# Kernel tuning notes

Measured on AMD Instinct MI355X. Metric: run time of the kernel, lower is better.

## Reference

```python
import jax, jax.numpy as jnp
import numpy as np

NUM_ITERS = 3

def squash(s, axis=-1):
    # standard capsule squash: ||s||^2/(1+||s||^2) * s/||s||
    sq = jnp.sum(s * s, axis=axis, keepdims=True)
    norm = jnp.sqrt(sq)
    return (sq / (1.0 + sq)) * (s / norm)

def setup_inputs() -> dict:
    key = jax.random.key(0)
    kx, kw = jax.random.split(key)
    B, I, k, l, O = 512, 1152, 8, 16, 7
    x = jax.random.normal(kx, (B, I, k), dtype=jnp.float32)
    w = jax.random.normal(kw, (I, k, l, O), dtype=jnp.float32)
    return {"x": x, "w": w}

def reference(x, w):
    # x: [B, I, k]; w: [I, k, l, O]
    u_hat = jnp.einsum('BIk,IklO->BIlO', x, w)            # [B, I, l, O]
    I, _, l, _ = w.shape
    b_ij = jnp.zeros((I, l), dtype=u_hat.dtype)
    v_j = None
    for _ in range(NUM_ITERS):
        c_ij = jax.nn.softmax(b_ij, axis=0)               # softmax over I
        s_j = jnp.einsum('Il,BIlO->BlO', c_ij, u_hat)     # [B, l, O]
        v_j = jnp.transpose(squash(s_j), (0, 2, 1))       # [B, O, l]
        u_vj = jnp.einsum('BOl,BIlO->BIl', v_j, u_hat).mean(axis=0)  # [I, l]
        b_ij = b_ij + u_vj
    return v_j
```

## Files before the change

kernel.cpp:

```cpp
#include <hip/hip_runtime.h>
#include <hip/hip_bf16.h>


#define NB 512
#define NI 1152
#define NLO 112
#define NIK 9216
#define NPAD 128

typedef __attribute__((ext_vector_type(8))) short bf16x8;
typedef __attribute__((ext_vector_type(4))) float f32x4;

__device__ __forceinline__ ushort f2bf(float f) {
    __hip_bfloat16 h = __float2bfloat16(f);
    return *(ushort*)&h;
}

__device__ __forceinline__ void conv_x_body(const float* __restrict__ x,
                                            ushort* __restrict__ xbf,
                                            ushort* __restrict__ xT, int bid) {
    __shared__ ushort tile[64][68];
    int kg = bid % 144, bg = bid / 144;
    int k0 = kg * 64, b0 = bg * 64;
    int t = threadIdx.x;
    for (int e = t; e < 1024; e += 256) {
        int r = e >> 4, c4 = (e & 15) * 4;
        float4 f = *(const float4*)&x[(size_t)(b0 + r) * NIK + k0 + c4];
        ushort4 u = { f2bf(f.x), f2bf(f.y), f2bf(f.z), f2bf(f.w) };
        *(ushort4*)&xbf[(size_t)(b0 + r) * NIK + k0 + c4] = u;
        tile[r][c4] = u.x; tile[r][c4 + 1] = u.y; tile[r][c4 + 2] = u.z; tile[r][c4 + 3] = u.w;
    }
    __syncthreads();
    for (int e = t; e < 1024; e += 256) {
        int kr = e >> 4, c4 = (e & 15) * 4;
        ushort4 u = { tile[c4][kr], tile[c4 + 1][kr], tile[c4 + 2][kr], tile[c4 + 3][kr] };
        *(ushort4*)&xT[(size_t)(k0 + kr) * NB + b0 + c4] = u;
    }
}

__global__ __launch_bounds__(256) void prep0(const float* __restrict__ x,
                                             ushort* __restrict__ xbf,
                                             ushort* __restrict__ xT,
                                             const float* __restrict__ w,
                                             ushort* __restrict__ wcTp,
                                             float* __restrict__ Z) {
    if (blockIdx.x < 1152) { conv_x_body(x, xbf, xT, blockIdx.x); return; }
    __shared__ ushort tile[NPAD][66];
    int t = threadIdx.x;
    int ik0 = (blockIdx.x - 1152) * 64;
    if (blockIdx.x == 1152 && t < 48) Z[t] = (t < 16) ? 1.0f : 0.0f;
    const float cv = 1.0f / 1152.0f;
    for (int e = t; e < 8192; e += 256) {
        int ikl = e >> 7, np = e & 127;
        int l = np >> 3, o = np & 7;
        float wv = (o < 7) ? w[(size_t)(ik0 + ikl) * NLO + l * 7 + o] : 0.f;
        tile[np][ikl] = f2bf(cv * wv);
    }
    __syncthreads();
    for (int e = t; e < 8192; e += 256) {
        int np = e >> 6, ikl = e & 63;
        wcTp[(size_t)np * NIK + ik0 + ikl] = tile[np][ikl];
    }
}

__global__ __launch_bounds__(1024) void sq_gemm(const ushort* __restrict__ xbf,
                                                const ushort* __restrict__ wcTp,
                                                const float* __restrict__ Zit,
                                                ushort* __restrict__ vT,
                                                float* __restrict__ out, int wout) {
    __shared__ float sp[16][16][16];
    __shared__ float ss[16][16];
    __shared__ float facs[16][2];
    __shared__ float zi[2];
    int bid = blockIdx.x;
    int mt = bid & 31, ng = bid >> 5;
    int b0 = mt * 16, n0 = ng * 16;
    int t = threadIdx.x;
    int wv = t >> 6, lane = t & 63;
    int row = lane & 15, quad = lane >> 4;
    int k0 = wv * 576;
    const ushort* ap = xbf + (size_t)(b0 + row) * NIK + k0 + quad * 8;
    const ushort* bp = wcTp + (size_t)(n0 + row) * NIK + k0 + quad * 8;
    f32x4 acc = {0.f, 0.f, 0.f, 0.f};
    #pragma unroll 6
    for (int ks = 0; ks < 18; ++ks) {
        bf16x8 a = *(const bf16x8*)(ap + ks * 32);
        bf16x8 b = *(const bf16x8*)(bp + ks * 32);
        acc = __builtin_amdgcn_mfma_f32_16x16x32_bf16(a, b, acc, 0, 0, 0);
    }
    if (t < 2) zi[t] = 1.0f / Zit[ng * 2 + t];
    #pragma unroll
    for (int r = 0; r < 4; ++r) sp[wv][quad * 4 + r][row] = acc[r];
    __syncthreads();
    if (t < 256) {
        int m = t >> 4, n = t & 15;
        float sv = 0.f;
        #pragma unroll
        for (int w8 = 0; w8 < 16; ++w8) sv += sp[w8][m][n];
        ss[m][n] = sv * zi[n >> 3];
    }
    __syncthreads();
    if (t < 32) {
        int m = t >> 1, ll = t & 1;
        float sq = 0.f;
        #pragma unroll
        for (int o = 0; o < 8; ++o) { float e = ss[m][ll * 8 + o]; sq += e * e; }
        facs[m][ll] = sqrtf(sq) / (1.0f + sq);
    }
    __syncthreads();
    if (t < 256) {
        int m = t >> 4, n = t & 15;
        int o = n & 7, lg = ng * 2 + (n >> 3);
        if (o < 7) {
            float vv = ss[m][n] * facs[m][n >> 3];
            vT[(size_t)(o * 16 + lg) * NB + b0 + m] = f2bf(vv);
            if (wout) out[(size_t)(b0 + m) * NLO + o * 16 + lg] = vv;
        }
    }
}

__global__ __launch_bounds__(512) void g_wc(const ushort* __restrict__ xT,
                                            const ushort* __restrict__ vT,
                                            const float* __restrict__ w,
                                            float* __restrict__ bij,
                                            ushort* __restrict__ wcTp,
                                            float* __restrict__ Zit, int accum) {
    __shared__ float bs[2][8][16];
    __shared__ float cs[128];
    __shared__ ushort tile[NPAD][66];
    int t = threadIdx.x;
    int wv = t >> 6;
    int lane = t & 63;
    int half = wv & 1;
    int mt = wv >> 1;
    int m0 = blockIdx.x * 64 + mt * 16;
    int kb0 = half * 256;
    int row = lane & 15, quad = lane >> 4;
    const ushort* ap = xT + (size_t)(m0 + row) * NB + kb0 + quad * 8;
    const ushort* bp = vT + (size_t)row * NB + kb0 + quad * 8;
    f32x4 acc[7];
    #pragma unroll
    for (int nt = 0; nt < 7; ++nt) acc[nt] = (f32x4){0.f, 0.f, 0.f, 0.f};
    #pragma unroll
    for (int ks = 0; ks < 8; ++ks) {
        bf16x8 a = *(const bf16x8*)(ap + ks * 32);
        #pragma unroll
        for (int nt = 0; nt < 7; ++nt) {
            bf16x8 bfr = *(const bf16x8*)(bp + (size_t)nt * 16 * NB + ks * 32);
            acc[nt] = __builtin_amdgcn_mfma_f32_16x16x32_bf16(a, bfr, acc[nt], 0, 0, 0);
        }
    }
    float S = 0.f;
    #pragma unroll
    for (int r = 0; r < 4; ++r) {
        int ik = m0 + quad * 4 + r;
        const float* wr = w + (size_t)ik * NLO + row * 7;
        float p = 0.f;
        #pragma unroll
        for (int o = 0; o < 7; ++o) p += wr[o] * acc[o][r];
        S += p;
    }
    float Sp = __shfl_down(S, 16);
    if ((quad & 1) == 0)
        bs[half][mt * 2 + (quad >> 1)][row] = (S + Sp) * (1.0f / 512.0f);
    __syncthreads();
    if (t < 128) {
        int il = t >> 4, l = t & 15;
        int i = blockIdx.x * 8 + il;
        float val = bs[0][il][l] + bs[1][il][l];
        if (accum) val += bij[i * 16 + l];
        bij[i * 16 + l] = val;
        cs[t] = expf(val);
    }
    __syncthreads();
    if (t < 16) {
        float z = 0.f;
        #pragma unroll
        for (int j = 0; j < 8; ++j) z += cs[j * 16 + t];
        atomicAdd(&Zit[t], z);
    }
    int ik0 = blockIdx.x * 64;
    for (int e = t; e < 8192; e += 512) {
        int ikl = e >> 7, np = e & 127;
        int l = np >> 3, o = np & 7;
        int il = ((ikl >> 3) << 4) + l;
        float wv_ = (o < 7) ? w[(size_t)(ik0 + ikl) * NLO + l * 7 + o] : 0.f;
        tile[np][ikl] = f2bf(cs[il] * wv_);
    }
    __syncthreads();
    for (int e = t; e < 8192; e += 512) {
        int np = e >> 6, ikl = e & 63;
        wcTp[(size_t)np * NIK + ik0 + ikl] = tile[np][ikl];
    }
}

extern "C" void kernel_launch(void* const* d_in, const int* in_sizes, int n_in,
                              void* d_out, int out_size, void* d_ws, size_t ws_size,
                              hipStream_t stream) {
    const float* x = (const float*)d_in[0];
    const float* w = (const float*)d_in[1];
    float* out = (float*)d_out;
    float* ws = (float*)d_ws;
    float*  f_bij  = ws;
    float*  f_Z    = f_bij + NI * 16;
    ushort* xbf    = (ushort*)(f_Z + 48);
    ushort* xT     = xbf + (size_t)NB * NIK;
    ushort* wcTp   = xT + (size_t)NIK * NB;
    ushort* vT     = wcTp + (size_t)NPAD * NIK;
    prep0<<<1296, 256, 0, stream>>>(x, xbf, xT, w, wcTp, f_Z);
    for (int it = 0; it < 3; ++it) {
        sq_gemm<<<256, 1024, 0, stream>>>(xbf, wcTp, f_Z + it * 16, vT, out,
                                          it == 2 ? 1 : 0);
        if (it < 2)
            g_wc<<<144, 512, 0, stream>>>(xT, vT, w, f_bij, wcTp,
                                          f_Z + (it + 1) * 16, it);
    }
}
```

Measured before the change: 178.4 us.

## Apply routing coefficients inside sq_gemm instead of rebuilding scaled weight matrix

Instead of g_wc rewriting a coefficient-scaled bf16 copy of the weights each iteration, the weights are transposed once to bf16, and g_wc only stores exp(b_ij). sq_gemm loads the per-row exp factors into shared memory and scales each weight fragment on the fly before the MFMA. This removes the per-iteration weight reload, scale and transposed write from g_wc. In exchange sq_gemm does extra unpack-multiply-repack ALU work and a shared-memory preload per block, and the unnormalised exp values feed into bf16 rounding (Z initialised to 1152 to compensate).

```diff
diff --git a/kernel.cpp b/kernel.cpp
--- a/kernel.cpp
+++ b/kernel.cpp
@@ -14,6 +14,11 @@
 __device__ __forceinline__ ushort f2bf(float f) {
     __hip_bfloat16 h = __float2bfloat16(f);
     return *(ushort*)&h;
+}
+__device__ __forceinline__ float bf2f(short s) {
+    union { unsigned int u; float f; } v;
+    v.u = ((unsigned int)(unsigned short)s) << 16;
+    return v.f;
 }
 
 __device__ __forceinline__ void conv_x_body(const float* __restrict__ x,
@@ -42,32 +47,36 @@
                                              ushort* __restrict__ xbf,
                                              ushort* __restrict__ xT,
                                              const float* __restrict__ w,
-                                             ushort* __restrict__ wcTp,
+                                             ushort* __restrict__ wpT,
+                                             float* __restrict__ eb,
                                              float* __restrict__ Z) {
     if (blockIdx.x < 1152) { conv_x_body(x, xbf, xT, blockIdx.x); return; }
     __shared__ ushort tile[NPAD][66];
     int t = threadIdx.x;
-    int ik0 = (blockIdx.x - 1152) * 64;
-    if (blockIdx.x == 1152 && t < 48) Z[t] = (t < 16) ? 1.0f : 0.0f;
-    const float cv = 1.0f / 1152.0f;
+    int wb = blockIdx.x - 1152;
+    int ik0 = wb * 64;
+    if (blockIdx.x == 1152 && t < 48) Z[t] = (t < 16) ? 1152.0f : 0.0f;
+    if (t < 128) eb[(size_t)(wb * 8 + (t >> 4)) * 16 + (t & 15)] = 1.0f;
     for (int e = t; e < 8192; e += 256) {
         int ikl = e >> 7, np = e & 127;
         int l = np >> 3, o = np & 7;
         float wv = (o < 7) ? w[(size_t)(ik0 + ikl) * NLO + l * 7 + o] : 0.f;
-        tile[np][ikl] = f2bf(cv * wv);
+        tile[np][ikl] = f2bf(wv);
     }
     __syncthreads();
     for (int e = t; e < 8192; e += 256) {
         int np = e >> 6, ikl = e & 63;
-        wcTp[(size_t)np * NIK + ik0 + ikl] = tile[np][ikl];
+        wpT[(size_t)np * NIK + ik0 + ikl] = tile[np][ikl];
     }
 }
 
 __global__ __launch_bounds__(1024) void sq_gemm(const ushort* __restrict__ xbf,
-                                                const ushort* __restrict__ wcTp,
+                                                const ushort* __restrict__ wpT,
+                                                const float* __restrict__ eb,
                                                 const float* __restrict__ Zit,
                                                 ushort* __restrict__ vT,
                                                 float* __restrict__ out, int wout) {
+    __shared__ float csl[NI * 2];
     __shared__ float sp[16][16][16];
     __shared__ float ss[16][16];
     __shared__ float facs[16][2];
@@ -79,16 +88,27 @@
     int wv = t >> 6, lane = t & 63;
     int row = lane & 15, quad = lane >> 4;
     int k0 = wv * 576;
+    for (int e = t; e < NI * 2; e += 1024) {
+        int i = e >> 1, ls = e & 1;
+        csl[e] = eb[(size_t)i * 16 + ng * 2 + ls];
+    }
+    if (t < 2) zi[t] = 1.0f / Zit[ng * 2 + t];
+    __syncthreads();
     const ushort* ap = xbf + (size_t)(b0 + row) * NIK + k0 + quad * 8;
-    const ushort* bp = wcTp + (size_t)(n0 + row) * NIK + k0 + quad * 8;
+    const ushort* bp = wpT + (size_t)(n0 + row) * NIK + k0 + quad * 8;
+    int lsel = row >> 3;
+    int i0 = (k0 >> 3) + quad;
     f32x4 acc = {0.f, 0.f, 0.f, 0.f};
     #pragma unroll 6
     for (int ks = 0; ks < 18; ++ks) {
         bf16x8 a = *(const bf16x8*)(ap + ks * 32);
-        bf16x8 b = *(const bf16x8*)(bp + ks * 32);
+        bf16x8 wf = *(const bf16x8*)(bp + ks * 32);
+        float cv = csl[(i0 + ks * 4) * 2 + lsel];
+        bf16x8 b;
+        #pragma unroll
+        for (int j = 0; j < 8; ++j) b[j] = (short)f2bf(bf2f(wf[j]) * cv);
         acc = __builtin_amdgcn_mfma_f32_16x16x32_bf16(a, b, acc, 0, 0, 0);
     }
-    if (t < 2) zi[t] = 1.0f / Zit[ng * 2 + t];
     #pragma unroll
     for (int r = 0; r < 4; ++r) sp[wv][quad * 4 + r][row] = acc[r];
     __syncthreads();
@@ -123,11 +143,10 @@
                                             const ushort* __restrict__ vT,
                                             const float* __restrict__ w,
                                             float* __restrict__ bij,
-                                            ushort* __restrict__ wcTp,
+                                            float* __restrict__ eb,
                                             float* __restrict__ Zit, int accum) {
     __shared__ float bs[2][8][16];
     __shared__ float cs[128];
-    __shared__ ushort tile[NPAD][66];
     int t = threadIdx.x;
     int wv = t >> 6;
     int lane = t & 63;
@@ -170,7 +189,9 @@
         float val = bs[0][il][l] + bs[1][il][l];
         if (accum) val += bij[i * 16 + l];
         bij[i * 16 + l] = val;
-        cs[t] = expf(val);
+        float e = expf(val);
+        cs[t] = e;
+        eb[(size_t)i * 16 + l] = e;
     }
     __syncthreads();
     if (t < 16) {
@@ -178,19 +199,6 @@
         #pragma unroll
         for (int j = 0; j < 8; ++j) z += cs[j * 16 + t];
         atomicAdd(&Zit[t], z);
-    }
-    int ik0 = blockIdx.x * 64;
-    for (int e = t; e < 8192; e += 512) {
-        int ikl = e >> 7, np = e & 127;
-        int l = np >> 3, o = np & 7;
-        int il = ((ikl >> 3) << 4) + l;
-        float wv_ = (o < 7) ? w[(size_t)(ik0 + ikl) * NLO + l * 7 + o] : 0.f;
-        tile[np][ikl] = f2bf(cs[il] * wv_);
-    }
-    __syncthreads();
-    for (int e = t; e < 8192; e += 512) {
-        int np = e >> 6, ikl = e & 63;
-        wcTp[(size_t)np * NIK + ik0 + ikl] = tile[np][ikl];
     }
 }
 
@@ -202,17 +210,18 @@
     float* out = (float*)d_out;
     float* ws = (float*)d_ws;
     float*  f_bij  = ws;
-    float*  f_Z    = f_bij + NI * 16;
+    float*  f_eb   = f_bij + NI * 16;
+    float*  f_Z    = f_eb + NI * 16;
     ushort* xbf    = (ushort*)(f_Z + 48);
     ushort* xT     = xbf + (size_t)NB * NIK;
-    ushort* wcTp   = xT + (size_t)NIK * NB;
-    ushort* vT     = wcTp + (size_t)NPAD * NIK;
-    prep0<<<1296, 256, 0, stream>>>(x, xbf, xT, w, wcTp, f_Z);
+    ushort* wpT    = xT + (size_t)NIK * NB;
+    ushort* vT     = wpT + (size_t)NPAD * NIK;
+    prep0<<<1296, 256, 0, stream>>>(x, xbf, xT, w, wpT, f_eb, f_Z);
     for (int it = 0; it < 3; ++it) {
-        sq_gemm<<<256, 1024, 0, stream>>>(xbf, wcTp, f_Z + it * 16, vT, out,
+        sq_gemm<<<256, 1024, 0, stream>>>(xbf, wpT, f_eb, f_Z + it * 16, vT, out,
                                           it == 2 ? 1 : 0);
         if (it < 2)
-            g_wc<<<144, 512, 0, stream>>>(xT, vT, w, f_bij, wcTp,
+            g_wc<<<144, 512, 0, stream>>>(xT, vT, w, f_bij, f_eb,
                                           f_Z + (it + 1) * 16, it);
     }
 }
```

Result: faster. 174.6 us (-2.1%).
